# Optimization experiments

Hardware: AMD Instinct MI355X
Metric: run time of the kernel (lower is better)

The kernel has to match this reference:

```python
import jax, jax.numpy as jnp
import numpy as np

N = 50000
E = 800000
D_IN = 128
HEADS = 2
C = 64  # per-head channels = out_channels // heads


def setup_inputs() -> dict:
    key = jax.random.key(0)
    ks = jax.random.split(key, 10)
    scale = 1.0 / np.sqrt(D_IN)
    x = jax.random.normal(ks[0], (N, D_IN), dtype=jnp.float32)
    edge_index = jax.random.randint(ks[1], (2, E), 0, N, dtype=jnp.int64)
    Wq = jax.random.normal(ks[2], (D_IN, HEADS * C), dtype=jnp.float32) * scale
    Wk = jax.random.normal(ks[3], (D_IN, HEADS * C), dtype=jnp.float32) * scale
    Wv = jax.random.normal(ks[4], (D_IN, HEADS * C), dtype=jnp.float32) * scale
    Wskip = jax.random.normal(ks[5], (D_IN, HEADS * C), dtype=jnp.float32) * scale
    bq = jnp.zeros((HEADS * C,), dtype=jnp.float32)
    bk = jnp.zeros((HEADS * C,), dtype=jnp.float32)
    bv = jnp.zeros((HEADS * C,), dtype=jnp.float32)
    bskip = jnp.zeros((HEADS * C,), dtype=jnp.float32)
    return {"x": x, "edge_index": edge_index, "Wq": Wq, "bq": bq,
            "Wk": Wk, "bk": bk, "Wv": Wv, "bv": bv,
            "Wskip": Wskip, "bskip": bskip}


def reference(x, edge_index, Wq, bq, Wk, bk, Wv, bv, Wskip, bskip):
    # TGATLayer.forward == TransformerConv (eval mode, dropout inactive),
    # concat=True, root_weight=True, beta=False, no edge_attr.
    n = x.shape[0]
    src, dst = edge_index[0], edge_index[1]  # messages flow src -> dst
    q = (x @ Wq + bq).reshape(n, HEADS, C)  # [N,H,C] query of destination
    k = (x @ Wk + bk).reshape(n, HEADS, C)  # [N,H,C] key of source
    v = (x @ Wv + bv).reshape(n, HEADS, C)  # [N,H,C] value of source
    # per-edge attention logits: (q_i . k_j) / sqrt(C)   -> [E,H]
    alpha = (q[dst] * k[src]).sum(-1) * (1.0 / np.sqrt(C)).astype(np.float32)
    # segment softmax over incoming edges of each destination node
    m = jax.ops.segment_max(alpha, dst, num_segments=n)          # [N,H]
    a = jnp.exp(alpha - m[dst])                                  # [E,H]
    denom = jax.ops.segment_sum(a, dst, num_segments=n)          # [N,H]
    # weighted scatter-add of values
    agg = jax.ops.segment_sum(a[:, :, None] * v[src], dst, num_segments=n)  # [N,H,C]
    agg = agg / jnp.maximum(denom, 1e-16)[:, :, None]
    out = agg.reshape(n, HEADS * C) + (x @ Wskip + bskip)  # concat heads + root skip
    return out
```

## Files before the change

kernel.cpp:

```cpp
#include <hip/hip_runtime.h>
#include <hip/hip_bf16.h>

typedef __attribute__((ext_vector_type(4))) float f32x4;
typedef __attribute__((ext_vector_type(8))) short bf16x8;

#define AS1 __attribute__((address_space(1)))
#define AS3 __attribute__((address_space(3)))
#define CAP 64

static __device__ __forceinline__ ushort f2bf(float v) {
    __hip_bfloat16 h = __float2bfloat16(v);
    return *reinterpret_cast<ushort*>(&h);
}
static __device__ __forceinline__ float bl(uint u) { return __uint_as_float(u << 16); }
static __device__ __forceinline__ float bh(uint u) { return __uint_as_float(u & 0xffff0000u); }
static __device__ __forceinline__ float bhr(uint u) { return __uint_as_float(u); }

__global__ __launch_bounds__(256) void prep_kernel(
    const float* __restrict__ Wq, const float* __restrict__ bq,
    const float* __restrict__ Wk, const float* __restrict__ bk,
    const float* __restrict__ Wv, const float* __restrict__ bv,
    const float* __restrict__ Ws, const float* __restrict__ bs,
    ushort* __restrict__ WcatT, float* __restrict__ bcat,
    const int* __restrict__ ei, int* __restrict__ count,
    int* __restrict__ sorted_src, int E_, int nHist)
{
    if ((int)blockIdx.x < nHist) {
        int e = (int)blockIdx.x * 256 + threadIdx.x;
        if (e < E_) {
            int s = ei[e];
            int d = ei[E_ + e];
            int rk = atomicAdd(&count[d], 1);
            if (rk < CAP) sorted_src[(d << 6) + rk] = s;
        }
        return;
    }
    int id = ((int)blockIdx.x - nHist) * 256 + threadIdx.x;
    int r = id >> 7, k = id & 127;
    int which, c;
    if (r < 128)      { which = 0; c = r; }
    else if (r < 384) { int j = r - 128; which = ((j & 3) < 2) ? 1 : 2;
                        c = ((j >> 2) << 1) + (j & 1); }
    else              { which = 3; c = r - 384; }
    const float* W = (which == 0) ? Wq : (which == 1) ? Wk : (which == 2) ? Wv : Ws;
    WcatT[(size_t)r * 128 + k] = f2bf(W[(size_t)k * 128 + c]);
    if (k == 0) {
        const float* b = (which == 0) ? bq : (which == 1) ? bk : (which == 2) ? bv : bs;
        bcat[r] = b[c];
    }
}

__global__ __launch_bounds__(256) void qkvs_mfma(
    const float* __restrict__ x, const ushort* __restrict__ WcatT,
    const float* __restrict__ bcat, ushort* __restrict__ yb, int n)
{
    __shared__ ushort smA[16384];

    const int t    = threadIdx.x;
    const int lane = t & 63;
    const int w    = t >> 6;
    const int wm   = w >> 1, wn = w & 1;
    const int row0 = blockIdx.x * 128;

    #pragma unroll
    for (int i = 0; i < 8; ++i) {
        int L = i * 256 + t;
        int r = L >> 4, ck = L & 15;
        int gr = min(row0 + r, n - 1);
        const float* gp = x + (size_t)gr * 128 + ck * 8;
        f32x4 lo = *reinterpret_cast<const f32x4*>(gp);
        f32x4 hi = *reinterpret_cast<const f32x4*>(gp + 4);
        uint4 o;
        o.x = (uint)f2bf(lo[0]) | ((uint)f2bf(lo[1]) << 16);
        o.y = (uint)f2bf(lo[2]) | ((uint)f2bf(lo[3]) << 16);
        o.z = (uint)f2bf(hi[0]) | ((uint)f2bf(hi[1]) << 16);
        o.w = (uint)f2bf(hi[2]) | ((uint)f2bf(hi[3]) << 16);
        *reinterpret_cast<uint4*>(smA + (size_t)r * 128 + ((ck ^ (r & 7)) << 3)) = o;
    }
    __syncthreads();

    #pragma unroll
    for (int ct = 0; ct < 4; ++ct) {
        f32x4 acc[4][4];
        #pragma unroll
        for (int i = 0; i < 4; ++i)
            #pragma unroll
            for (int j = 0; j < 4; ++j) acc[i][j] = (f32x4)(0.f);

        #pragma unroll
        for (int kb = 0; kb < 4; ++kb) {
            bf16x8 a[4], b[4];
            #pragma unroll
            for (int cn = 0; cn < 4; ++cn) {
                int wcol = ct * 128 + wn * 64 + cn * 16 + (lane & 15);
                b[cn] = *reinterpret_cast<const bf16x8*>(
                    WcatT + (size_t)wcol * 128 + kb * 32 + (lane >> 4) * 8);
            }
            #pragma unroll
            for (int rm = 0; rm < 4; ++rm) {
                int r  = wm * 64 + rm * 16 + (lane & 15);
                int ck = (kb * 4 + (lane >> 4)) ^ (r & 7);
                a[rm] = *reinterpret_cast<const bf16x8*>(smA + (size_t)r * 128 + ck * 8);
            }
            #pragma unroll
            for (int rm = 0; rm < 4; ++rm)
                #pragma unroll
                for (int cn = 0; cn < 4; ++cn)
                    acc[rm][cn] = __builtin_amdgcn_mfma_f32_16x16x32_bf16(
                        b[cn], a[rm], acc[rm][cn], 0, 0, 0);
        }

        #pragma unroll
        for (int rm = 0; rm < 4; ++rm) {
            int gr = row0 + wm * 64 + rm * 16 + (lane & 15);
            if (gr < n) {
                #pragma unroll
                for (int cn = 0; cn < 4; ++cn) {
                    int nb = wn * 64 + cn * 16 + (lane >> 4) * 4;
                    f32x4 bb = *reinterpret_cast<const f32x4*>(bcat + ct * 128 + nb);
                    f32x4 v  = acc[rm][cn];
                    uint2 o;
                    o.x = (uint)f2bf(v[0] + bb[0]) | ((uint)f2bf(v[1] + bb[1]) << 16);
                    o.y = (uint)f2bf(v[2] + bb[2]) | ((uint)f2bf(v[3] + bb[3]) << 16);
                    *reinterpret_cast<uint2*>(yb + (size_t)gr * 512 + ct * 128 + nb) = o;
                }
            }
        }
    }
}

static __device__ __forceinline__ float dotp(const float q[8], uint4 A, uint4 B) {
    return q[0]*bl(A.x) + q[1]*bhr(A.x) + q[2]*bl(A.z) + q[3]*bhr(A.z)
         + q[4]*bl(B.x) + q[5]*bhr(B.x) + q[6]*bl(B.z) + q[7]*bhr(B.z);
}
static __device__ __forceinline__ void accum(float (&acc)[8], float& den,
                                             float a, uint4 A, uint4 B) {
    den += a;
    acc[0] += a*bl(A.y); acc[1] += a*bhr(A.y); acc[2] += a*bl(A.w); acc[3] += a*bhr(A.w);
    acc[4] += a*bl(B.y); acc[5] += a*bhr(B.y); acc[6] += a*bl(B.w); acc[7] += a*bhr(B.w);
}

__global__ __launch_bounds__(256) void node_agg(
    const uint* __restrict__ yb32, const int* __restrict__ count,
    const int* __restrict__ sorted_src, float* __restrict__ out, int n)
{
    const int node = blockIdx.x * 4 + (threadIdx.x >> 6);
    const int lane = threadIdx.x & 63;
    if (node >= n) return;
    const int g  = lane >> 4;
    const int il = lane & 15;

    const uint* row = yb32 + (size_t)node * 256;
    const uint4 qv = *reinterpret_cast<const uint4*>(row + 4 * il);
    const int   sidx = sorted_src[((size_t)node << 6) + lane];
    float q[8] = { bl(qv.x)*0.125f, bh(qv.x)*0.125f, bl(qv.y)*0.125f, bh(qv.y)*0.125f,
                   bl(qv.z)*0.125f, bh(qv.z)*0.125f, bl(qv.w)*0.125f, bh(qv.w)*0.125f };

    const int deg = min(count[node], CAP);

    float acc[8] = {0.f,0.f,0.f,0.f,0.f,0.f,0.f,0.f};
    float den = 0.f;

    int e = 0;
    for (; e + 8 <= deg; e += 8) {
        const int sA = __shfl(sidx, e + g, 64);
        const int sB = __shfl(sidx, e + 4 + g, 64);
        const uint* pa = yb32 + (size_t)sA * 256 + 64 + 8 * il;
        const uint* pb = yb32 + (size_t)sB * 256 + 64 + 8 * il;
        uint4 Aa = *reinterpret_cast<const uint4*>(pa);
        uint4 Ba = *reinterpret_cast<const uint4*>(pa + 4);
        uint4 Ab = *reinterpret_cast<const uint4*>(pb);
        uint4 Bb = *reinterpret_cast<const uint4*>(pb + 4);
        float p1 = dotp(q, Aa, Ba);
        float p2 = dotp(q, Ab, Bb);
        p1 += __shfl_xor(p1, 1, 64);  p2 += __shfl_xor(p2, 1, 64);
        p1 += __shfl_xor(p1, 2, 64);  p2 += __shfl_xor(p2, 2, 64);
        p1 += __shfl_xor(p1, 4, 64);  p2 += __shfl_xor(p2, 4, 64);
        float a1 = __expf(p1), a2 = __expf(p2);
        accum(acc, den, a1, Aa, Ba);
        accum(acc, den, a2, Ab, Bb);
    }
    for (; e < deg; e += 4) {
        const int idx = e + g;
        const bool act = idx < deg;
        const int s = __shfl(sidx, act ? idx : 0, 64);
        const uint* pa = yb32 + (size_t)s * 256 + 64 + 8 * il;
        uint4 A = *reinterpret_cast<const uint4*>(pa);
        uint4 B = *reinterpret_cast<const uint4*>(pa + 4);
        float p = dotp(q, A, B);
        p += __shfl_xor(p, 1, 64);
        p += __shfl_xor(p, 2, 64);
        p += __shfl_xor(p, 4, 64);
        float a = act ? __expf(p) : 0.f;
        accum(acc, den, a, A, B);
    }

    #pragma unroll
    for (int j = 0; j < 8; ++j) {
        acc[j] += __shfl_xor(acc[j], 16, 64);
        acc[j] += __shfl_xor(acc[j], 32, 64);
    }
    den += __shfl_xor(den, 16, 64);
    den += __shfl_xor(den, 32, 64);

    if (lane < 16) {
        const float inv = 1.f / fmaxf(den, 1e-16f);
        const uint4 sv = *reinterpret_cast<const uint4*>(row + 192 + 4 * il);
        f32x4 o0, o1;
        o0[0] = acc[0]*inv + bl(sv.x);  o0[1] = acc[1]*inv + bh(sv.x);
        o0[2] = acc[2]*inv + bl(sv.y);  o0[3] = acc[3]*inv + bh(sv.y);
        o1[0] = acc[4]*inv + bl(sv.z);  o1[1] = acc[5]*inv + bh(sv.z);
        o1[2] = acc[6]*inv + bl(sv.w);  o1[3] = acc[7]*inv + bh(sv.w);
        float* op = out + (size_t)node * 128 + 8 * il;
        *reinterpret_cast<f32x4*>(op)     = o0;
        *reinterpret_cast<f32x4*>(op + 4) = o1;
    }
}

extern "C" void kernel_launch(void* const* d_in, const int* in_sizes, int n_in,
                              void* d_out, int out_size, void* d_ws, size_t ws_size,
                              hipStream_t stream) {
    const float* x  = (const float*)d_in[0];
    const int*   ei = (const int*)d_in[1];
    const float* Wq = (const float*)d_in[2];
    const float* bq = (const float*)d_in[3];
    const float* Wk = (const float*)d_in[4];
    const float* bk = (const float*)d_in[5];
    const float* Wv = (const float*)d_in[6];
    const float* bv = (const float*)d_in[7];
    const float* Ws = (const float*)d_in[8];
    const float* bs = (const float*)d_in[9];

    const int N = in_sizes[0] / 128;
    const int E = in_sizes[1] / 2;

    ushort* yb    = (ushort*)d_ws;
    ushort* WcatT = yb + (size_t)N * 512;
    float*  bcat  = (float*)(WcatT + 512 * 128);
    int* count      = (int*)(bcat + 512);
    int* sorted_src = count + N;
    float* out      = (float*)d_out;

    hipMemsetAsync(count, 0, (size_t)N * sizeof(int), stream);

    const int nHist = (E + 255) / 256;
    prep_kernel<<<nHist + 256, 256, 0, stream>>>(
        Wq, bq, Wk, bk, Wv, bv, Ws, bs, WcatT, bcat, ei, count, sorted_src, E, nHist);

    qkvs_mfma<<<(N + 127) / 128, 256, 0, stream>>>(x, WcatT, bcat, yb, N);

    node_agg<<<(N + 3) / 4, 256, 0, stream>>>((const uint*)yb, count, sorted_src, out, N);
}
```

Before: 147.1 us.

## Fuse count zeroing into weight prep, merge histogram with MFMA projection

Replaces the memset and the prep kernel with a setup kernel that zeroes the per-node counts and builds the transposed bf16 weights. A second kernel runs the edge bucketing and the QKV/skip MFMA projection as disjoint block ranges of one launch, so they can overlap. The aggregation kernel now reads source indices directly from memory instead of through a wave-wide register and shuffle. This removes launch and serialization overhead, but the bucketing blocks now carry the GEMM's large shared-memory allocation, which can lower their occupancy.

```diff
diff --git a/kernel.cpp b/kernel.cpp
--- a/kernel.cpp
+++ b/kernel.cpp
@@ -16,17 +16,47 @@
 static __device__ __forceinline__ float bh(uint u) { return __uint_as_float(u & 0xffff0000u); }
 static __device__ __forceinline__ float bhr(uint u) { return __uint_as_float(u); }
 
-__global__ __launch_bounds__(256) void prep_kernel(
+__global__ __launch_bounds__(256) void setup_zero(
     const float* __restrict__ Wq, const float* __restrict__ bq,
     const float* __restrict__ Wk, const float* __restrict__ bk,
     const float* __restrict__ Wv, const float* __restrict__ bv,
     const float* __restrict__ Ws, const float* __restrict__ bs,
     ushort* __restrict__ WcatT, float* __restrict__ bcat,
+    int* __restrict__ count, int n)
+{
+    const int bid = blockIdx.x;
+    if (bid < 256) {
+        int id = bid * 256 + threadIdx.x;
+        int r = id >> 7, k = id & 127;
+        int which, c;
+        if (r < 128)      { which = 0; c = r; }
+        else if (r < 384) { int j = r - 128; which = ((j & 3) < 2) ? 1 : 2;
+                            c = ((j >> 2) << 1) + (j & 1); }
+        else              { which = 3; c = r - 384; }
+        const float* W = (which == 0) ? Wq : (which == 1) ? Wk : (which == 2) ? Wv : Ws;
+        WcatT[(size_t)r * 128 + k] = f2bf(W[(size_t)k * 128 + c]);
+        if (k == 0) {
+            const float* b = (which == 0) ? bq : (which == 1) ? bk : (which == 2) ? bv : bs;
+            bcat[r] = b[c];
+        }
+    } else {
+        int i = (bid - 256) * 256 + threadIdx.x;
+        if (i < n) count[i] = 0;
+    }
+}
+
+__global__ __launch_bounds__(256) void mid_kernel(
+    const float* __restrict__ x, const ushort* __restrict__ WcatT,
+    const float* __restrict__ bcat, ushort* __restrict__ yb, int n,
     const int* __restrict__ ei, int* __restrict__ count,
     int* __restrict__ sorted_src, int E_, int nHist)
 {
+    __shared__ ushort smA[16384];
+
+    const int t = threadIdx.x;
+
     if ((int)blockIdx.x < nHist) {
-        int e = (int)blockIdx.x * 256 + threadIdx.x;
+        int e = (int)blockIdx.x * 256 + t;
         if (e < E_) {
             int s = ei[e];
             int d = ei[E_ + e];
@@ -35,32 +65,11 @@
         }
         return;
     }
-    int id = ((int)blockIdx.x - nHist) * 256 + threadIdx.x;
-    int r = id >> 7, k = id & 127;
-    int which, c;
-    if (r < 128)      { which = 0; c = r; }
-    else if (r < 384) { int j = r - 128; which = ((j & 3) < 2) ? 1 : 2;
-                        c = ((j >> 2) << 1) + (j & 1); }
-    else              { which = 3; c = r - 384; }
-    const float* W = (which == 0) ? Wq : (which == 1) ? Wk : (which == 2) ? Wv : Ws;
-    WcatT[(size_t)r * 128 + k] = f2bf(W[(size_t)k * 128 + c]);
-    if (k == 0) {
-        const float* b = (which == 0) ? bq : (which == 1) ? bk : (which == 2) ? bv : bs;
-        bcat[r] = b[c];
-    }
-}
-
-__global__ __launch_bounds__(256) void qkvs_mfma(
-    const float* __restrict__ x, const ushort* __restrict__ WcatT,
-    const float* __restrict__ bcat, ushort* __restrict__ yb, int n)
-{
-    __shared__ ushort smA[16384];
-
-    const int t    = threadIdx.x;
+
     const int lane = t & 63;
     const int w    = t >> 6;
     const int wm   = w >> 1, wn = w & 1;
-    const int row0 = blockIdx.x * 128;
+    const int row0 = ((int)blockIdx.x - nHist) * 128;
 
     #pragma unroll
     for (int i = 0; i < 8; ++i) {
@@ -152,19 +161,18 @@
 
     const uint* row = yb32 + (size_t)node * 256;
     const uint4 qv = *reinterpret_cast<const uint4*>(row + 4 * il);
-    const int   sidx = sorted_src[((size_t)node << 6) + lane];
     float q[8] = { bl(qv.x)*0.125f, bh(qv.x)*0.125f, bl(qv.y)*0.125f, bh(qv.y)*0.125f,
                    bl(qv.z)*0.125f, bh(qv.z)*0.125f, bl(qv.w)*0.125f, bh(qv.w)*0.125f };
 
     const int deg = min(count[node], CAP);
+    const int* sp = sorted_src + ((size_t)node << 6);
 
     float acc[8] = {0.f,0.f,0.f,0.f,0.f,0.f,0.f,0.f};
     float den = 0.f;
 
     int e = 0;
     for (; e + 8 <= deg; e += 8) {
-        const int sA = __shfl(sidx, e + g, 64);
-        const int sB = __shfl(sidx, e + 4 + g, 64);
+        const int sA = sp[e + g], sB = sp[e + 4 + g];
         const uint* pa = yb32 + (size_t)sA * 256 + 64 + 8 * il;
         const uint* pb = yb32 + (size_t)sB * 256 + 64 + 8 * il;
         uint4 Aa = *reinterpret_cast<const uint4*>(pa);
@@ -183,7 +191,7 @@
     for (; e < deg; e += 4) {
         const int idx = e + g;
         const bool act = idx < deg;
-        const int s = __shfl(sidx, act ? idx : 0, 64);
+        const int s = sp[act ? idx : deg - 1];
         const uint* pa = yb32 + (size_t)s * 256 + 64 + 8 * il;
         uint4 A = *reinterpret_cast<const uint4*>(pa);
         uint4 B = *reinterpret_cast<const uint4*>(pa + 4);
@@ -241,13 +249,14 @@
     int* sorted_src = count + N;
     float* out      = (float*)d_out;
 
-    hipMemsetAsync(count, 0, (size_t)N * sizeof(int), stream);
+    const int zeroBlocks = (N + 255) / 256;
+    setup_zero<<<256 + zeroBlocks, 256, 0, stream>>>(
+        Wq, bq, Wk, bk, Wv, bv, Ws, bs, WcatT, bcat, count, N);
 
     const int nHist = (E + 255) / 256;
-    prep_kernel<<<nHist + 256, 256, 0, stream>>>(
-        Wq, bq, Wk, bk, Wv, bv, Ws, bs, WcatT, bcat, ei, count, sorted_src, E, nHist);
-
-    qkvs_mfma<<<(N + 127) / 128, 256, 0, stream>>>(x, WcatT, bcat, yb, N);
+    const int nMfma = (N + 127) / 128;
+    mid_kernel<<<nHist + nMfma, 256, 0, stream>>>(
+        x, WcatT, bcat, yb, N, ei, count, sorted_src, E, nHist);
 
     node_agg<<<(N + 3) / 4, 256, 0, stream>>>((const uint*)yb, count, sorted_src, out, N);
 }
```

Measured after the change: 171.7 us. 1.17x slower.
